# Performance work log

Measured on AMD Instinct MI355X. Metric: run time of the kernel, lower is better.

The kernel has to match this reference:

```python
import jax, jax.numpy as jnp
import numpy as np

B, LQ, LK, D = 16, 2048, 2048, 64
TEMPERATURE = 8.0  # sqrt(d_k)


def setup_inputs() -> dict:
    key = jax.random.key(0)
    kq, kk, kv, km = jax.random.split(key, 4)
    q = jax.random.normal(kq, (B, LQ, D), dtype=jnp.float32)
    k = jax.random.normal(kk, (B, LK, D), dtype=jnp.float32)
    v = jax.random.normal(kv, (B, LK, D), dtype=jnp.float32)
    mask = jax.random.randint(km, (B, LQ, LK), 0, 2).astype(jnp.bool_)
    return {"q": q, "k": k, "v": v, "mask": mask}


def reference(q, k, v, mask):
    # attn = bmm(q, k^T) / temperature  -> [B, LQ, LK]
    attn = jnp.einsum("bqd,bkd->bqk", q, k) / TEMPERATURE
    attn = jnp.where(mask, -jnp.inf, attn)
    attn = jax.nn.softmax(attn, axis=2)
    out = jnp.einsum("bqk,bkd->bqd", attn, v)  # [B, LQ, D]
    return out, attn
```

## Files before the change

### kernel.cpp

```cpp
#include <hip/hip_runtime.h>

namespace {
constexpr int kB = 16;
constexpr int kLQ = 2048;
constexpr int kLK = 2048;
constexpr int kD = 64;
constexpr int kQBlk = 16;
constexpr int kStride = 2056;
}

using short8 = __attribute__((ext_vector_type(8))) short;
using f32x4 = __attribute__((ext_vector_type(4))) float;

static __device__ __forceinline__ unsigned short f2bf(float x) {
    unsigned u = __builtin_bit_cast(unsigned, x);
    u += 0x7FFFu + ((u >> 16) & 1u);
    return (unsigned short)(u >> 16);
}
static __device__ __forceinline__ float bf2f(unsigned short s) {
    unsigned u = ((unsigned)s) << 16;
    return __builtin_bit_cast(float, u);
}
static __device__ __forceinline__ short8 cvt8(float4 a, float4 b, float s) {
    return short8{(short)f2bf(a.x*s), (short)f2bf(a.y*s), (short)f2bf(a.z*s), (short)f2bf(a.w*s),
                  (short)f2bf(b.x*s), (short)f2bf(b.y*s), (short)f2bf(b.z*s), (short)f2bf(b.w*s)};
}

__global__ __launch_bounds__(512, 4) void sdpa_v3_kernel(
    const float* __restrict__ qg, const float* __restrict__ kg,
    const float* __restrict__ vg, const void* __restrict__ maskg,
    float* __restrict__ outg, float* __restrict__ attng)
{
    __shared__ unsigned short s_s[kQBlk][kStride];
    __shared__ float s_wsum[8][16];
    __shared__ float s_red[kQBlk][kD];
    __shared__ int s_flag;

    const int tid = threadIdx.x;
    const int wave = tid >> 6;
    const int lane = tid & 63;
    const int r16 = lane & 15;
    const int g = lane >> 4;

    const int blk = blockIdx.x;
    const int b = blk >> 7;
    const int qrow0 = (blk & 127) * kQBlk;

    if (tid < 64) {
        unsigned w = ((const unsigned*)maskg)[tid];
        unsigned long long bal = __ballot((w & 0xFFFFFF00u) != 0u);
        if (tid == 0) s_flag = (bal != 0ull) ? 1 : 0;
    }
    __syncthreads();
    const bool mask_byte = (s_flag != 0);
    const unsigned char* mask_u8 = (const unsigned char*)maskg;
    const int* mask_i32 = (const int*)maskg;

    short8 q0, q1;
    {
        const float4* qp = (const float4*)(qg + ((size_t)b * kLQ + qrow0 + r16) * kD);
        float4 x0 = qp[2*g + 0], x1 = qp[2*g + 1];
        float4 x2 = qp[2*g + 8], x3 = qp[2*g + 9];
        q0 = cvt8(x0, x1, 0.125f);
        q1 = cvt8(x2, x3, 0.125f);
    }
    const size_t kbase = (size_t)b * kLK * kD;
    const size_t mrowL = ((size_t)b * kLQ + qrow0 + r16) * (size_t)kLK;
    float wsum = 0.f;

    for (int t = wave; t < kLK / 32; t += 8) {
        const int col0 = t * 32;
        const float4* kpA = (const float4*)(kg + kbase + (size_t)(col0 + r16) * kD);
        const float4* kpB = (const float4*)(kg + kbase + (size_t)(col0 + 16 + r16) * kD);
        float4 a0 = kpA[2*g + 0], a1 = kpA[2*g + 1], a2 = kpA[2*g + 8], a3 = kpA[2*g + 9];
        float4 c0 = kpB[2*g + 0], c1 = kpB[2*g + 1], c2 = kpB[2*g + 8], c3 = kpB[2*g + 9];
        short8 kA0 = cvt8(a0, a1, 1.f), kA1 = cvt8(a2, a3, 1.f);
        short8 kB0 = cvt8(c0, c1, 1.f), kB1 = cvt8(c2, c3, 1.f);
        f32x4 accA = {0.f, 0.f, 0.f, 0.f}, accB = {0.f, 0.f, 0.f, 0.f};
        accA = __builtin_amdgcn_mfma_f32_16x16x32_bf16(kA0, q0, accA, 0, 0, 0);
        accA = __builtin_amdgcn_mfma_f32_16x16x32_bf16(kA1, q1, accA, 0, 0, 0);
        accB = __builtin_amdgcn_mfma_f32_16x16x32_bf16(kB0, q0, accB, 0, 0, 0);
        accB = __builtin_amdgcn_mfma_f32_16x16x32_bf16(kB1, q1, accB, 0, 0, 0);

        const int cA = col0 + 4*g;
        const int cB = col0 + 16 + 4*g;
        float eA[4], eB[4];
        if (mask_byte) {
            const unsigned mwA = *(const unsigned*)(mask_u8 + mrowL + cA);
            const unsigned mwB = *(const unsigned*)(mask_u8 + mrowL + cB);
#pragma unroll
            for (int r = 0; r < 4; ++r) {
                eA[r] = ((mwA >> (8*r)) & 0xFFu) ? 0.f : __expf(accA[r]);
                eB[r] = ((mwB >> (8*r)) & 0xFFu) ? 0.f : __expf(accB[r]);
            }
        } else {
            const int4 mwA = *(const int4*)(mask_i32 + mrowL + cA);
            const int4 mwB = *(const int4*)(mask_i32 + mrowL + cB);
            eA[0] = mwA.x ? 0.f : __expf(accA[0]);
            eA[1] = mwA.y ? 0.f : __expf(accA[1]);
            eA[2] = mwA.z ? 0.f : __expf(accA[2]);
            eA[3] = mwA.w ? 0.f : __expf(accA[3]);
            eB[0] = mwB.x ? 0.f : __expf(accB[0]);
            eB[1] = mwB.y ? 0.f : __expf(accB[1]);
            eB[2] = mwB.z ? 0.f : __expf(accB[2]);
            eB[3] = mwB.w ? 0.f : __expf(accB[3]);
        }
        wsum += (eA[0] + eA[1]) + (eA[2] + eA[3]) + (eB[0] + eB[1]) + (eB[2] + eB[3]);
        const unsigned long long pA = (unsigned long long)f2bf(eA[0])
                                    | ((unsigned long long)f2bf(eA[1]) << 16)
                                    | ((unsigned long long)f2bf(eA[2]) << 32)
                                    | ((unsigned long long)f2bf(eA[3]) << 48);
        const unsigned long long pB = (unsigned long long)f2bf(eB[0])
                                    | ((unsigned long long)f2bf(eB[1]) << 16)
                                    | ((unsigned long long)f2bf(eB[2]) << 32)
                                    | ((unsigned long long)f2bf(eB[3]) << 48);
        *(unsigned long long*)&s_s[r16][cA] = pA;
        *(unsigned long long*)&s_s[r16][cB] = pB;
    }
    wsum += __shfl_xor(wsum, 16, 64);
    wsum += __shfl_xor(wsum, 32, 64);
    if (g == 0) s_wsum[wave][r16] = wsum;
    __syncthreads();

    {
        const int rr = tid >> 5;
        const int cc = tid & 31;
        float rsum = 0.f;
#pragma unroll
        for (int w = 0; w < 8; ++w) rsum += s_wsum[w][rr];
        const float rinv = 1.0f / rsum;
        float* arow = attng + ((size_t)b * kLQ + qrow0 + rr) * kLK;
#pragma unroll 4
        for (int i = 0; i < 16; ++i) {
            const int col = cc * 4 + i * 128;
            const unsigned long long sv = *(const unsigned long long*)&s_s[rr][col];
            float4 a;
            a.x = bf2f((unsigned short)(sv >>  0)) * rinv;
            a.y = bf2f((unsigned short)(sv >> 16)) * rinv;
            a.z = bf2f((unsigned short)(sv >> 32)) * rinv;
            a.w = bf2f((unsigned short)(sv >> 48)) * rinv;
            *(float4*)(arow + col) = a;
        }
    }

    {
        const int d0 = (wave & 3) * 16;
        const int kh = wave >> 2;
        const float* vbase = vg + (size_t)b * kLK * kD + d0 + r16;
        f32x4 acc = {0.f, 0.f, 0.f, 0.f};
#pragma unroll 2
        for (int kt = kh * 32; kt < kh * 32 + 32; ++kt) {
            const int kk0 = kt * 32 + 8 * g;
            const short8 af = *(const short8*)&s_s[r16][kk0];
            float v0 = vbase[(size_t)(kk0 + 0) * kD], v1 = vbase[(size_t)(kk0 + 1) * kD];
            float v2 = vbase[(size_t)(kk0 + 2) * kD], v3 = vbase[(size_t)(kk0 + 3) * kD];
            float v4 = vbase[(size_t)(kk0 + 4) * kD], v5 = vbase[(size_t)(kk0 + 5) * kD];
            float v6 = vbase[(size_t)(kk0 + 6) * kD], v7 = vbase[(size_t)(kk0 + 7) * kD];
            const short8 bv = short8{(short)f2bf(v0), (short)f2bf(v1), (short)f2bf(v2), (short)f2bf(v3),
                                     (short)f2bf(v4), (short)f2bf(v5), (short)f2bf(v6), (short)f2bf(v7)};
            acc = __builtin_amdgcn_mfma_f32_16x16x32_bf16(af, bv, acc, 0, 0, 0);
        }
        if (kh == 1) {
#pragma unroll
            for (int r = 0; r < 4; ++r) s_red[4*g + r][d0 + r16] = acc[r];
        }
        __syncthreads();
        if (kh == 0) {
#pragma unroll
            for (int r = 0; r < 4; ++r) {
                const int m = 4*g + r;
                float rs = 0.f;
#pragma unroll
                for (int w = 0; w < 8; ++w) rs += s_wsum[w][m];
                outg[((size_t)b * kLQ + qrow0 + m) * kD + d0 + r16] =
                    (acc[r] + s_red[m][d0 + r16]) * (1.0f / rs);
            }
        }
    }
}

extern "C" void kernel_launch(void* const* d_in, const int* in_sizes, int n_in,
                              void* d_out, int out_size, void* d_ws, size_t ws_size,
                              hipStream_t stream) {
    (void)in_sizes; (void)n_in; (void)out_size; (void)d_ws; (void)ws_size;
    const float* q = (const float*)d_in[0];
    const float* k = (const float*)d_in[1];
    const float* v = (const float*)d_in[2];
    const void* mask = d_in[3];
    float* out = (float*)d_out;
    float* attn = out + (size_t)kB * kLQ * kD;
    const dim3 grid(kB * (kLQ / kQBlk));
    sdpa_v3_kernel<<<grid, 512, 0, stream>>>(q, k, v, mask, out, attn);
}
```

Measured before the change: 271.4 us.

## Software-pipeline K/V loads, prefetch mask, use exp2 and packed bf16 conversion

```diff
diff --git a/kernel.cpp b/kernel.cpp
--- a/kernel.cpp
+++ b/kernel.cpp
@@ -1,4 +1,5 @@
 #include <hip/hip_runtime.h>
+#include <hip/hip_bf16.h>
 
 namespace {
 constexpr int kB = 16;
@@ -7,26 +8,32 @@
 constexpr int kD = 64;
 constexpr int kQBlk = 16;
 constexpr int kStride = 2056;
+constexpr float kLog2e = 1.44269504088896340736f;
 }
 
 using short8 = __attribute__((ext_vector_type(8))) short;
 using f32x4 = __attribute__((ext_vector_type(4))) float;
 
-static __device__ __forceinline__ unsigned short f2bf(float x) {
-    unsigned u = __builtin_bit_cast(unsigned, x);
-    u += 0x7FFFu + ((u >> 16) & 1u);
-    return (unsigned short)(u >> 16);
+union S8U { short8 v; unsigned u[4]; unsigned long long q[2]; };
+
+static __device__ __forceinline__ unsigned pk2(float lo, float hi) {
+    __hip_bfloat162 h = __float22bfloat162_rn(float2{lo, hi});
+    unsigned short a = __builtin_bit_cast(unsigned short, h.x);
+    unsigned short b = __builtin_bit_cast(unsigned short, h.y);
+    return (unsigned)a | ((unsigned)b << 16);
 }
 static __device__ __forceinline__ float bf2f(unsigned short s) {
     unsigned u = ((unsigned)s) << 16;
     return __builtin_bit_cast(float, u);
 }
-static __device__ __forceinline__ short8 cvt8(float4 a, float4 b, float s) {
-    return short8{(short)f2bf(a.x*s), (short)f2bf(a.y*s), (short)f2bf(a.z*s), (short)f2bf(a.w*s),
-                  (short)f2bf(b.x*s), (short)f2bf(b.y*s), (short)f2bf(b.z*s), (short)f2bf(b.w*s)};
-}
-
-__global__ __launch_bounds__(512, 4) void sdpa_v3_kernel(
+static __device__ __forceinline__ short8 cvt8(float4 a, float4 b) {
+    S8U r;
+    r.u[0] = pk2(a.x, a.y); r.u[1] = pk2(a.z, a.w);
+    r.u[2] = pk2(b.x, b.y); r.u[3] = pk2(b.z, b.w);
+    return r.v;
+}
+
+__global__ __launch_bounds__(512, 4) void sdpa_v5_kernel(
     const float* __restrict__ qg, const float* __restrict__ kg,
     const float* __restrict__ vg, const void* __restrict__ maskg,
     float* __restrict__ outg, float* __restrict__ attng)
@@ -59,23 +66,50 @@
     short8 q0, q1;
     {
         const float4* qp = (const float4*)(qg + ((size_t)b * kLQ + qrow0 + r16) * kD);
+        const float s = 0.125f * kLog2e;
         float4 x0 = qp[2*g + 0], x1 = qp[2*g + 1];
         float4 x2 = qp[2*g + 8], x3 = qp[2*g + 9];
-        q0 = cvt8(x0, x1, 0.125f);
-        q1 = cvt8(x2, x3, 0.125f);
+        x0 *= s; x1 *= s; x2 *= s; x3 *= s;
+        q0 = cvt8(x0, x1);
+        q1 = cvt8(x2, x3);
     }
     const size_t kbase = (size_t)b * kLK * kD;
     const size_t mrowL = ((size_t)b * kLQ + qrow0 + r16) * (size_t)kLK;
     float wsum = 0.f;
 
-    for (int t = wave; t < kLK / 32; t += 8) {
-        const int col0 = t * 32;
+    unsigned hmA[8], hmB[8];
+    if (mask_byte) {
+#pragma unroll
+        for (int i = 0; i < 8; ++i) {
+            const int c0 = (wave + 8 * i) * 32;
+            hmA[i] = *(const unsigned*)(mask_u8 + mrowL + c0 + 4*g);
+            hmB[i] = *(const unsigned*)(mask_u8 + mrowL + c0 + 16 + 4*g);
+        }
+    }
+
+    float4 cur[8], nxt[8];
+    {
+        const int col0 = wave * 32;
         const float4* kpA = (const float4*)(kg + kbase + (size_t)(col0 + r16) * kD);
         const float4* kpB = (const float4*)(kg + kbase + (size_t)(col0 + 16 + r16) * kD);
-        float4 a0 = kpA[2*g + 0], a1 = kpA[2*g + 1], a2 = kpA[2*g + 8], a3 = kpA[2*g + 9];
-        float4 c0 = kpB[2*g + 0], c1 = kpB[2*g + 1], c2 = kpB[2*g + 8], c3 = kpB[2*g + 9];
-        short8 kA0 = cvt8(a0, a1, 1.f), kA1 = cvt8(a2, a3, 1.f);
-        short8 kB0 = cvt8(c0, c1, 1.f), kB1 = cvt8(c2, c3, 1.f);
+        cur[0] = kpA[2*g]; cur[1] = kpA[2*g+1]; cur[2] = kpA[2*g+8]; cur[3] = kpA[2*g+9];
+        cur[4] = kpB[2*g]; cur[5] = kpB[2*g+1]; cur[6] = kpB[2*g+8]; cur[7] = kpB[2*g+9];
+    }
+#pragma unroll
+    for (int i = 0; i < 8; ++i) {
+        const int t = wave + 8 * i;
+        const int col0 = t * 32;
+        if (i < 7) {
+            const int nc0 = (t + 8) * 32;
+            const float4* kpA = (const float4*)(kg + kbase + (size_t)(nc0 + r16) * kD);
+            const float4* kpB = (const float4*)(kg + kbase + (size_t)(nc0 + 16 + r16) * kD);
+            nxt[0] = kpA[2*g]; nxt[1] = kpA[2*g+1]; nxt[2] = kpA[2*g+8]; nxt[3] = kpA[2*g+9];
+            nxt[4] = kpB[2*g]; nxt[5] = kpB[2*g+1]; nxt[6] = kpB[2*g+8]; nxt[7] = kpB[2*g+9];
+        }
+        const short8 kA0 = cvt8(cur[0], cur[1]);
+        const short8 kA1 = cvt8(cur[2], cur[3]);
+        const short8 kB0 = cvt8(cur[4], cur[5]);
+        const short8 kB1 = cvt8(cur[6], cur[7]);
         f32x4 accA = {0.f, 0.f, 0.f, 0.f}, accB = {0.f, 0.f, 0.f, 0.f};
         accA = __builtin_amdgcn_mfma_f32_16x16x32_bf16(kA0, q0, accA, 0, 0, 0);
         accA = __builtin_amdgcn_mfma_f32_16x16x32_bf16(kA1, q1, accA, 0, 0, 0);
@@ -84,38 +118,29 @@
 
         const int cA = col0 + 4*g;
         const int cB = col0 + 16 + 4*g;
+        unsigned mwA, mwB;
+        if (mask_byte) {
+            mwA = hmA[i]; mwB = hmB[i];
+        } else {
+            const int4 a = *(const int4*)(mask_i32 + mrowL + cA);
+            const int4 c = *(const int4*)(mask_i32 + mrowL + cB);
+            mwA = (a.x ? 1u : 0u) | (a.y ? 0x100u : 0u) | (a.z ? 0x10000u : 0u) | (a.w ? 0x1000000u : 0u);
+            mwB = (c.x ? 1u : 0u) | (c.y ? 0x100u : 0u) | (c.z ? 0x10000u : 0u) | (c.w ? 0x1000000u : 0u);
+        }
         float eA[4], eB[4];
-        if (mask_byte) {
-            const unsigned mwA = *(const unsigned*)(mask_u8 + mrowL + cA);
-            const unsigned mwB = *(const unsigned*)(mask_u8 + mrowL + cB);
-#pragma unroll
-            for (int r = 0; r < 4; ++r) {
-                eA[r] = ((mwA >> (8*r)) & 0xFFu) ? 0.f : __expf(accA[r]);
-                eB[r] = ((mwB >> (8*r)) & 0xFFu) ? 0.f : __expf(accB[r]);
-            }
-        } else {
-            const int4 mwA = *(const int4*)(mask_i32 + mrowL + cA);
-            const int4 mwB = *(const int4*)(mask_i32 + mrowL + cB);
-            eA[0] = mwA.x ? 0.f : __expf(accA[0]);
-            eA[1] = mwA.y ? 0.f : __expf(accA[1]);
-            eA[2] = mwA.z ? 0.f : __expf(accA[2]);
-            eA[3] = mwA.w ? 0.f : __expf(accA[3]);
-            eB[0] = mwB.x ? 0.f : __expf(accB[0]);
-            eB[1] = mwB.y ? 0.f : __expf(accB[1]);
-            eB[2] = mwB.z ? 0.f : __expf(accB[2]);
-            eB[3] = mwB.w ? 0.f : __expf(accB[3]);
+#pragma unroll
+        for (int r = 0; r < 4; ++r) {
+            eA[r] = ((mwA >> (8*r)) & 0xFFu) ? 0.f : __builtin_amdgcn_exp2f(accA[r]);
+            eB[r] = ((mwB >> (8*r)) & 0xFFu) ? 0.f : __builtin_amdgcn_exp2f(accB[r]);
         }
         wsum += (eA[0] + eA[1]) + (eA[2] + eA[3]) + (eB[0] + eB[1]) + (eB[2] + eB[3]);
-        const unsigned long long pA = (unsigned long long)f2bf(eA[0])
-                                    | ((unsigned long long)f2bf(eA[1]) << 16)
-                                    | ((unsigned long long)f2bf(eA[2]) << 32)
-                                    | ((unsigned long long)f2bf(eA[3]) << 48);
-        const unsigned long long pB = (unsigned long long)f2bf(eB[0])
-                                    | ((unsigned long long)f2bf(eB[1]) << 16)
-                                    | ((unsigned long long)f2bf(eB[2]) << 32)
-                                    | ((unsigned long long)f2bf(eB[3]) << 48);
-        *(unsigned long long*)&s_s[r16][cA] = pA;
-        *(unsigned long long*)&s_s[r16][cB] = pB;
+        S8U pA, pB;
+        pA.u[0] = pk2(eA[0], eA[1]); pA.u[1] = pk2(eA[2], eA[3]);
+        pB.u[0] = pk2(eB[0], eB[1]); pB.u[1] = pk2(eB[2], eB[3]);
+        *(unsigned long long*)&s_s[r16][cA] = pA.q[0];
+        *(unsigned long long*)&s_s[r16][cB] = pB.q[0];
+#pragma unroll
+        for (int j = 0; j < 8; ++j) cur[j] = nxt[j];
     }
     wsum += __shfl_xor(wsum, 16, 64);
     wsum += __shfl_xor(wsum, 32, 64);
@@ -128,7 +153,7 @@
         float rsum = 0.f;
 #pragma unroll
         for (int w = 0; w < 8; ++w) rsum += s_wsum[w][rr];
-        const float rinv = 1.0f / rsum;
+        const float rinv = __builtin_amdgcn_rcpf(rsum);
         float* arow = attng + ((size_t)b * kLQ + qrow0 + rr) * kLK;
 #pragma unroll 4
         for (int i = 0; i < 16; ++i) {
@@ -147,18 +172,24 @@
         const int d0 = (wave & 3) * 16;
         const int kh = wave >> 2;
         const float* vbase = vg + (size_t)b * kLK * kD + d0 + r16;
+        float va[8], vb[8];
+#pragma unroll
+        for (int j = 0; j < 8; ++j) va[j] = vbase[(size_t)(kh*1024 + 8*g + j) * kD];
         f32x4 acc = {0.f, 0.f, 0.f, 0.f};
-#pragma unroll 2
-        for (int kt = kh * 32; kt < kh * 32 + 32; ++kt) {
-            const int kk0 = kt * 32 + 8 * g;
+#pragma unroll
+        for (int kt = 0; kt < 32; ++kt) {
+            const int kk0 = (kh * 32 + kt) * 32 + 8 * g;
+            float* cv = (kt & 1) ? vb : va;
+            float* nv = (kt & 1) ? va : vb;
+            if (kt < 31) {
+#pragma unroll
+                for (int j = 0; j < 8; ++j) nv[j] = vbase[(size_t)(kk0 + 32 + j) * kD];
+            }
             const short8 af = *(const short8*)&s_s[r16][kk0];
-            float v0 = vbase[(size_t)(kk0 + 0) * kD], v1 = vbase[(size_t)(kk0 + 1) * kD];
-            float v2 = vbase[(size_t)(kk0 + 2) * kD], v3 = vbase[(size_t)(kk0 + 3) * kD];
-            float v4 = vbase[(size_t)(kk0 + 4) * kD], v5 = vbase[(size_t)(kk0 + 5) * kD];
-            float v6 = vbase[(size_t)(kk0 + 6) * kD], v7 = vbase[(size_t)(kk0 + 7) * kD];
-            const short8 bv = short8{(short)f2bf(v0), (short)f2bf(v1), (short)f2bf(v2), (short)f2bf(v3),
-                                     (short)f2bf(v4), (short)f2bf(v5), (short)f2bf(v6), (short)f2bf(v7)};
-            acc = __builtin_amdgcn_mfma_f32_16x16x32_bf16(af, bv, acc, 0, 0, 0);
+            S8U bv;
+            bv.u[0] = pk2(cv[0], cv[1]); bv.u[1] = pk2(cv[2], cv[3]);
+            bv.u[2] = pk2(cv[4], cv[5]); bv.u[3] = pk2(cv[6], cv[7]);
+            acc = __builtin_amdgcn_mfma_f32_16x16x32_bf16(af, bv.v, acc, 0, 0, 0);
         }
         if (kh == 1) {
 #pragma unroll
@@ -173,7 +204,7 @@
 #pragma unroll
                 for (int w = 0; w < 8; ++w) rs += s_wsum[w][m];
                 outg[((size_t)b * kLQ + qrow0 + m) * kD + d0 + r16] =
-                    (acc[r] + s_red[m][d0 + r16]) * (1.0f / rs);
+                    (acc[r] + s_red[m][d0 + r16]) * __builtin_amdgcn_rcpf(rs);
             }
         }
     }
@@ -190,5 +221,5 @@
     float* out = (float*)d_out;
     float* attn = out + (size_t)kB * kLQ * kD;
     const dim3 grid(kB * (kLQ / kQBlk));
-    sdpa_v3_kernel<<<grid, 512, 0, stream>>>(q, k, v, mask, out, attn);
-}
+    sdpa_v5_kernel<<<grid, 512, 0, stream>>>(q, k, v, mask, out, attn);
+}
```

New measurement: 278.1 us. +2.5%, slower.
